# Optimization experiments

Hardware: AMD Instinct MI355X
Metric: run time of the kernel (lower is better)

## Reference

```python
import jax, jax.numpy as jnp
import numpy as np

N, E = 100000, 3200000
F_IN, H, ED, C = 21, 64, 3, 2
EPS = 1e-5


def setup_inputs() -> dict:
    key = jax.random.key(0)
    ks = jax.random.split(key, 20)
    def lin(k, fan_out, fan_in):
        s = 1.0 / np.sqrt(fan_in)
        return jax.random.uniform(k, (fan_out, fan_in), jnp.float32, -s, s)
    inp = {
        'x': jax.random.normal(ks[0], (N, F_IN), jnp.float32),
        'edge_index': jax.random.randint(ks[1], (2, E), 0, N, jnp.int64),
        'edge_attr': jax.random.normal(ks[2], (E, ED), jnp.float32),
        # edge encoder Linear(ED -> H)
        'We': lin(ks[3], H, ED), 'be': jnp.zeros((H,), jnp.float32),
        # conv1 SAGEConv(F_IN -> H): lin_l (neighbors, with bias), lin_r (root, no bias)
        'W1l': lin(ks[4], H, F_IN), 'b1l': jnp.zeros((H,), jnp.float32),
        'W1r': lin(ks[5], H, F_IN),
        # conv2 SAGEConv(H -> H)
        'W2l': lin(ks[6], H, H), 'b2l': jnp.zeros((H,), jnp.float32),
        'W2r': lin(ks[7], H, H),
        # BatchNorms
        'g1': jnp.ones((H,), jnp.float32), 'beta1': jnp.zeros((H,), jnp.float32),
        'g2': jnp.ones((H,), jnp.float32), 'beta2': jnp.zeros((H,), jnp.float32),
        # classifier Linear(H -> C)
        'Wc': lin(ks[8], C, H), 'bc': jnp.zeros((C,), jnp.float32),
    }
    return inp


def _bn(h, g, b):
    # training-mode BatchNorm1d: batch stats, biased variance
    mu = jnp.mean(h, axis=0)
    var = jnp.mean(jnp.square(h - mu), axis=0)
    return (h - mu) * jax.lax.rsqrt(var + EPS) * g + b


def reference(x, edge_index, edge_attr, We, be, W1l, b1l, W1r, W2l, b2l, W2r,
              g1, beta1, g2, beta2, Wc, bc):
    n = x.shape[0]
    src, dst = edge_index[0], edge_index[1]
    # degree (in-degree at target), clamped to 1 for mean aggregation
    deg = jax.ops.segment_sum(jnp.ones((src.shape[0],), x.dtype), dst, num_segments=n)
    inv_deg = (1.0 / jnp.maximum(deg, 1.0))[:, None]  # [N,1]

    def sage(h, Wl, bl, Wr):
        agg = jax.ops.segment_sum(h[src], dst, num_segments=n) * inv_deg  # mean over in-neighbors
        return agg @ Wl.T + bl + h @ Wr.T

    # edge feature encoding + scatter-add to target nodes
    edge_enc = jax.nn.relu(edge_attr @ We.T + be)                # [E,H]
    edge_agg = jax.ops.segment_sum(edge_enc, dst, num_segments=n)  # [N,H]

    h = sage(x, W1l, b1l, W1r) + edge_agg
    h = jax.nn.relu(_bn(h, g1, beta1))
    # dropout omitted (deterministic reference)
    h = sage(h, W2l, b2l, W2r)
    h = jax.nn.relu(_bn(h, g2, beta2))
    return h @ Wc.T + bc  # logits [N,2]
```

## Files before the change

### kernel.cpp

```cpp
#include <hip/hip_runtime.h>
#include <hip/hip_fp16.h>

#define NN 100000
#define NE 3200000
#define F_IN 21
#define HID 64
#define EPS 1e-5f

#define NB 1000
#define BN 100
#define SCAP 3712
#define AB 256
#define AEPB 12500


__global__ void __launch_bounds__(256) kC1_slab_r14(
    const int* __restrict__ src, const int* __restrict__ dst,
    const float* __restrict__ eattr,
    int* __restrict__ segStart, int* __restrict__ btot,
    float4* __restrict__ packB, unsigned char* __restrict__ dlArr) {
    __shared__ int lcnt[NB];
    __shared__ int lpart[256];
    __shared__ int lcur[NB];
    int tid = threadIdx.x;
    for (int i = tid; i < NB; i += 256) lcnt[i] = 0;
    __syncthreads();
    int base = blockIdx.x * AEPB;
    for (int k = tid; k < AEPB; k += 256) atomicAdd(&lcnt[dst[base + k] / BN], 1);
    __syncthreads();
    int mySum = 0;
    if (tid < 250)
        mySum = lcnt[4 * tid] + lcnt[4 * tid + 1] + lcnt[4 * tid + 2] + lcnt[4 * tid + 3];
    lpart[tid] = mySum;
    __syncthreads();
    for (int off = 1; off < 256; off <<= 1) {
        int v = (tid >= off) ? lpart[tid - off] : 0;
        __syncthreads();
        lpart[tid] += v;
        __syncthreads();
    }
    if (tid < 250) {
        int run = lpart[tid] - mySum;
#pragma unroll
        for (int j = 0; j < 4; ++j) {
            int b = 4 * tid + j;
            int c = lcnt[b];
            int st = base + run;
            lcur[b] = st;
            segStart[b * AB + blockIdx.x] = st;
            if (c) atomicAdd(&btot[b], c);
            run += c;
        }
    }
    if (tid == 0) segStart[NB * AB + blockIdx.x] = base + AEPB;
    __syncthreads();
    for (int k = tid; k < AEPB; k += 256) {
        int e = base + k;
        int d = dst[e];
        int b = d / BN;
        int dl = d - b * BN;
        int pos = atomicAdd(&lcur[b], 1);
        size_t eb = (size_t)e * 3;
        float4 pk = {__int_as_float(src[e] | (dl << 17)),
                     eattr[eb], eattr[eb + 1], eattr[eb + 2]};
        packB[pos] = pk;
        dlArr[pos] = (unsigned char)dl;
    }
}

__global__ void kB2_scan_r14(const int* __restrict__ btot, int* __restrict__ bucketBase,
                             int* __restrict__ rowptr) {
    __shared__ int lds[1024];
    int t = threadIdx.x;
    int v = (t < NB) ? btot[t] : 0;
    lds[t] = v;
    __syncthreads();
    for (int off = 1; off < 1024; off <<= 1) {
        int u = (t >= off) ? lds[t - off] : 0;
        __syncthreads();
        lds[t] += u;
        __syncthreads();
    }
    if (t < NB) bucketBase[t] = lds[t] - v;
    if (t == 0) rowptr[NN] = NE;
}

__global__ void kP_pad_r14(const float* __restrict__ x, __half* __restrict__ xh) {
    int i = blockIdx.x * blockDim.x + threadIdx.x;
    int st = gridDim.x * blockDim.x;
    for (; i < NN * 32; i += st) {
        int n = i >> 5, c = i & 31;
        xh[i] = __float2half((c < F_IN) ? x[(size_t)n * F_IN + c] : 0.f);
    }
}


#define R3X(v) { v += __shfl_xor(v, 8); v += __shfl_xor(v, 16); v += __shfl_xor(v, 32); }
#define R2X(v) { v += __shfl_xor(v, 16); v += __shfl_xor(v, 32); }
#define PICK(v, kk) ((kk) == 0 ? (v).x : (kk) == 1 ? (v).y : (kk) == 2 ? (v).z : (v).w)

__global__ void __launch_bounds__(512, 1) kFuse_r14(
    const float4* __restrict__ packB, const unsigned char* __restrict__ dlArr,
    const int* __restrict__ segStart, const int* __restrict__ bucketBase,
    const __half* __restrict__ xh, const float* __restrict__ x,
    const float* __restrict__ We, const float* __restrict__ be,
    const float* __restrict__ W1l, const float* __restrict__ b1l,
    const float* __restrict__ W1r,
    float* __restrict__ H1, int* __restrict__ csr_src, int* __restrict__ rowptr,
    float* __restrict__ gsum, float* __restrict__ gsq) {
    __shared__ float4 stage[SCAP];
    __shared__ int segA[AB], segL[AB];
    __shared__ int lcnt2[BN], lofs[BN], lcur2[BN];
    __shared__ float eLds[8 * HID];
    __shared__ float bs[HID], bq[HID];
    int tid = threadIdx.x;
    int b = blockIdx.x;
    int base = bucketBase[b];
    if (tid < AB) {
        int a = segStart[b * AB + tid];
        segA[tid] = a;
        segL[tid] = segStart[(b + 1) * AB + tid] - a;
    }
    for (int i = tid; i < BN; i += 512) lcnt2[i] = 0;
    if (tid < HID) { bs[tid] = 0.f; bq[tid] = 0.f; }
    __syncthreads();
    int lane = tid & 63, wid = tid >> 6;
    for (int s = wid; s < AB; s += 8) {
        int L = segL[s], A = segA[s];
        for (int i = lane; i < L; i += 64) atomicAdd(&lcnt2[dlArr[A + i]], 1);
    }
    __syncthreads();
    if (tid == 0) {
        int run = 0;
        for (int d = 0; d < BN; ++d) { lofs[d] = run; lcur2[d] = run; run += lcnt2[d]; }
    }
    __syncthreads();
    if (tid < BN) rowptr[b * BN + tid] = base + lofs[tid];
    for (int s = wid; s < AB; s += 8) {
        int L = segL[s], A = segA[s];
        for (int i = lane; i < L; i += 64) {
            float4 pk = packB[A + i];
            int dl = __float_as_int(pk.x) >> 17;
            int pos = atomicAdd(&lcur2[dl], 1);
            if (pos < SCAP) stage[pos] = pk;
        }
    }
    __syncthreads();
    int cntB = lofs[BN - 1] + lcnt2[BN - 1];
    int lim = min(cntB, SCAP);
    for (int i = tid; i < lim; i += 512)
        csr_src[base + i] = __float_as_int(stage[i].x) & 0x1FFFF;
    int g = lane >> 3, q = lane & 7;
    float w0[8], w1[8], w2[8], bqv[8];
#pragma unroll
    for (int r = 0; r < 8; ++r) {
        int ch = 8 * q + r;
        w0[r] = We[ch * 3]; w1[r] = We[ch * 3 + 1]; w2[r] = We[ch * 3 + 2];
        bqv[r] = be[ch];
    }
    float wl[F_IN], wr[F_IN];
#pragma unroll
    for (int k = 0; k < F_IN; ++k) {
        wl[k] = W1l[lane * F_IN + k];
        wr[k] = W1r[lane * F_IN + k];
    }
    float b1 = b1l[lane];
    float psum = 0.f, psq = 0.f;
    for (int d = wid; d < BN; d += 8) {
        int lbeg = lofs[d];
        int deg = lcnt2[d];
        int lend = lbeg + deg;
        float aX0 = 0, aX1 = 0, aX2 = 0, aX3 = 0;
        float aE[8] = {0, 0, 0, 0, 0, 0, 0, 0};
        for (int i0 = lbeg + g; i0 < lend; i0 += 32) {
            uint2 xv[4];
            float4 pk_[4];
            float mk[4];
#pragma unroll
            for (int u = 0; u < 4; ++u) {
                int i = i0 + u * 8;
                mk[u] = (i < lend) ? 1.f : 0.f;
                int ic = min(min(i, lend - 1), SCAP - 1);
                float4 pk = stage[ic];
                pk_[u] = pk;
                int s = __float_as_int(pk.x) & 0x1FFFF;
                xv[u] = *(const uint2*)(xh + (size_t)s * 32 + 4 * q);
            }
#pragma unroll
            for (int u = 0; u < 4; ++u) {
                float2 f0 = __half22float2(*(__half2*)&xv[u].x);
                float2 f1 = __half22float2(*(__half2*)&xv[u].y);
                float m = mk[u];
                aX0 = fmaf(f0.x, m, aX0);
                aX1 = fmaf(f0.y, m, aX1);
                aX2 = fmaf(f1.x, m, aX2);
                aX3 = fmaf(f1.y, m, aX3);
#pragma unroll
                for (int r = 0; r < 8; ++r) {
                    float e = fmaf(w0[r], pk_[u].y,
                              fmaf(w1[r], pk_[u].z, fmaf(w2[r], pk_[u].w, bqv[r])));
                    aE[r] = fmaf(fmaxf(e, 0.f), m, aE[r]);
                }
            }
        }
        R3X(aX0) R3X(aX1) R3X(aX2) R3X(aX3)
#pragma unroll
        for (int r = 0; r < 8; ++r) { R3X(aE[r]) }
        if (g == 0) {
            float4 e0 = {aE[0], aE[1], aE[2], aE[3]};
            float4 e1 = {aE[4], aE[5], aE[6], aE[7]};
            *(float4*)(eLds + wid * HID + 8 * q) = e0;
            *(float4*)(eLds + wid * HID + 8 * q + 4) = e1;
        }
        int n = b * BN + d;
        float4 aXq = {aX0, aX1, aX2, aX3};
        float xv = (lane < F_IN) ? x[(size_t)n * F_IN + lane] : 0.f;
        float own = b1, agg = 0.f;
#pragma unroll
        for (int k = 0; k < F_IN; ++k) {
            own = fmaf(wr[k], __shfl(xv, k), own);
            agg = fmaf(wl[k], __shfl(PICK(aXq, k & 3), k >> 2), agg);
        }
        float invd = 1.f / fmaxf((float)deg, 1.f);
        float h = own + agg * invd + eLds[wid * HID + lane];
        H1[(size_t)n * HID + lane] = h;
        psum += h; psq += h * h;
    }
    atomicAdd(&bs[lane], psum);
    atomicAdd(&bq[lane], psq);
    __syncthreads();
    if (tid < HID) {
        atomicAdd(&gsum[tid], bs[tid]);
        atomicAdd(&gsq[tid], bq[tid]);
    }
}

__global__ void kG_bnstat_r14(const float* __restrict__ gsum, const float* __restrict__ gsq,
                              const float* __restrict__ g, const float* __restrict__ beta,
                              float* __restrict__ scale, float* __restrict__ shift) {
    int c = threadIdx.x;
    if (c < HID) {
        float mu = gsum[c] * (1.f / (float)NN);
        float var = gsq[c] * (1.f / (float)NN) - mu * mu;
        float rstd = rsqrtf(var + EPS);
        float sc = rstd * g[c];
        scale[c] = sc;
        shift[c] = beta[c] - mu * sc;
    }
}

__global__ void kAct_r14(const float* __restrict__ H1,
                         const float* __restrict__ sc1, const float* __restrict__ sh1,
                         __half* __restrict__ act) {
    int i = blockIdx.x * blockDim.x + threadIdx.x;
    int st = gridDim.x * blockDim.x;
    for (; i < NN * HID; i += st) {
        int c = i & 63;
        act[i] = __float2half(fmaxf(fmaf(H1[i], sc1[c], sh1[c]), 0.f));
    }
}


__global__ void __launch_bounds__(256, 2) kG2f_r14(
    const __half* __restrict__ act, const int* __restrict__ csr_src,
    const int* __restrict__ rowptr,
    const float* __restrict__ W2l, const float* __restrict__ W2r,
    const float* __restrict__ b2l,
    float* __restrict__ h2, float* __restrict__ gsum, float* __restrict__ gsq) {
    __shared__ float ldsL[HID * HID];
    __shared__ float ldsR[HID * HID];
    __shared__ float bs[HID], bq[HID];
    for (int i = threadIdx.x; i < HID * HID; i += blockDim.x) {
        int k = i >> 6, c = i & 63;
        ldsL[i] = W2l[c * HID + k];
        ldsR[i] = W2r[c * HID + k];
    }
    if (threadIdx.x < HID) { bs[threadIdx.x] = 0.f; bq[threadIdx.x] = 0.f; }
    __syncthreads();
    int lane = threadIdx.x & 63;
    int g = lane >> 4, c4 = lane & 15;
    float b2 = b2l[lane];
    int gw = blockIdx.x * 4 + (threadIdx.x >> 6);
    int nw = gridDim.x * 4;
    float psum = 0.f, psq = 0.f;
    for (int n = gw; n < NN; n += nw) {
        int beg = rowptr[n], end = rowptr[n + 1];
        int deg = end - beg;
        float a0 = 0, a1 = 0, a2 = 0, a3 = 0;
        for (int p0 = beg; p0 < end; p0 += 64) {
            int cnt = min(64, end - p0);
            int sL = (lane < cnt) ? csr_src[p0 + lane] : 0;
            int jm = (cnt + 3) >> 2;
            for (int jb = 0; jb < jm; jb += 8) {
                uint2 v[8];
                float mk[8];
#pragma unroll
                for (int u = 0; u < 8; ++u) {
                    int idx = (jb + u) * 4 + g;
                    int s = __shfl(sL, idx);
                    mk[u] = (idx < cnt) ? 1.f : 0.f;
                    v[u] = *(const uint2*)(act + (size_t)s * HID + 4 * c4);
                }
#pragma unroll
                for (int u = 0; u < 8; ++u) {
                    float2 f0 = __half22float2(*(__half2*)&v[u].x);
                    float2 f1 = __half22float2(*(__half2*)&v[u].y);
                    float m = mk[u];
                    a0 = fmaf(f0.x, m, a0);
                    a1 = fmaf(f0.y, m, a1);
                    a2 = fmaf(f1.x, m, a2);
                    a3 = fmaf(f1.y, m, a3);
                }
            }
        }
        R2X(a0) R2X(a1) R2X(a2) R2X(a3)
        float invd = 1.f / fmaxf((float)deg, 1.f);
        float4 aq = {a0 * invd, a1 * invd, a2 * invd, a3 * invd};
        float v2 = __half2float(act[(size_t)n * HID + lane]);
        float o0 = b2, o1 = 0.f, o2 = 0.f, o3 = 0.f;
#pragma unroll
        for (int k = 0; k < HID; k += 4) {
            float va0 = __shfl(PICK(aq, k & 3), k >> 2);
            float vb0 = __shfl(v2, k);
            o0 = fmaf(ldsL[k * HID + lane], va0, fmaf(ldsR[k * HID + lane], vb0, o0));
            float va1 = __shfl(PICK(aq, (k + 1) & 3), (k + 1) >> 2);
            float vb1 = __shfl(v2, k + 1);
            o1 = fmaf(ldsL[(k + 1) * HID + lane], va1, fmaf(ldsR[(k + 1) * HID + lane], vb1, o1));
            float va2 = __shfl(PICK(aq, (k + 2) & 3), (k + 2) >> 2);
            float vb2 = __shfl(v2, k + 2);
            o2 = fmaf(ldsL[(k + 2) * HID + lane], va2, fmaf(ldsR[(k + 2) * HID + lane], vb2, o2));
            float va3 = __shfl(PICK(aq, (k + 3) & 3), (k + 3) >> 2);
            float vb3 = __shfl(v2, k + 3);
            o3 = fmaf(ldsL[(k + 3) * HID + lane], va3, fmaf(ldsR[(k + 3) * HID + lane], vb3, o3));
        }
        float o = (o0 + o1) + (o2 + o3);
        h2[(size_t)n * HID + lane] = o;
        psum += o; psq += o * o;
    }
    atomicAdd(&bs[lane], psum);
    atomicAdd(&bq[lane], psq);
    __syncthreads();
    if (threadIdx.x < HID) {
        atomicAdd(&gsum[threadIdx.x], bs[threadIdx.x]);
        atomicAdd(&gsq[threadIdx.x], bq[threadIdx.x]);
    }
}


__global__ void kJ_out_r14(const float* __restrict__ H2,
                           const float* __restrict__ sc2, const float* __restrict__ sh2,
                           const float* __restrict__ Wc, const float* __restrict__ bc,
                           float* __restrict__ out) {
    int lane = threadIdx.x & 63;
    int g = lane >> 4, c4 = lane & 15;
    int wv = blockIdx.x * 4 + (threadIdx.x >> 6);
    int nw = gridDim.x * 4;
    float4 sc = *(const float4*)(sc2 + 4 * c4);
    float4 sh = *(const float4*)(sh2 + 4 * c4);
    float4 w0 = *(const float4*)(Wc + 4 * c4);
    float4 w1 = *(const float4*)(Wc + HID + 4 * c4);
    float b0 = bc[0], b1 = bc[1];
    for (int t = wv; t < NN / 4; t += nw) {
        int n = t * 4 + g;
        float4 h = *(const float4*)(H2 + (size_t)n * HID + 4 * c4);
        float vx = fmaxf(fmaf(h.x, sc.x, sh.x), 0.f);
        float vy = fmaxf(fmaf(h.y, sc.y, sh.y), 0.f);
        float vz = fmaxf(fmaf(h.z, sc.z, sh.z), 0.f);
        float vw = fmaxf(fmaf(h.w, sc.w, sh.w), 0.f);
        float r0 = vx * w0.x + vy * w0.y + vz * w0.z + vw * w0.w;
        float r1 = vx * w1.x + vy * w1.y + vz * w1.z + vw * w1.w;
#pragma unroll
        for (int off = 1; off <= 8; off <<= 1) {
            r0 += __shfl_xor(r0, off);
            r1 += __shfl_xor(r1, off);
        }
        if (c4 == 0) {
            out[(size_t)n * 2] = r0 + b0;
            out[(size_t)n * 2 + 1] = r1 + b1;
        }
    }
}


extern "C" void kernel_launch(void* const* d_in, const int* in_sizes, int n_in,
                              void* d_out, int out_size, void* d_ws, size_t ws_size,
                              hipStream_t stream) {
    const float* x = (const float*)d_in[0];
    const int* ei = (const int*)d_in[1];
    const float* eattr = (const float*)d_in[2];
    const float* We = (const float*)d_in[3];
    const float* be = (const float*)d_in[4];
    const float* W1l = (const float*)d_in[5];
    const float* b1l = (const float*)d_in[6];
    const float* W1r = (const float*)d_in[7];
    const float* W2l = (const float*)d_in[8];
    const float* b2l = (const float*)d_in[9];
    const float* W2r = (const float*)d_in[10];
    const float* g1 = (const float*)d_in[11];
    const float* beta1 = (const float*)d_in[12];
    const float* g2 = (const float*)d_in[13];
    const float* beta2 = (const float*)d_in[14];
    const float* Wc = (const float*)d_in[15];
    const float* bc = (const float*)d_in[16];
    float* out = (float*)d_out;

    const int* e_src = ei;
    const int* e_dst = ei + NE;

    char* ws = (char*)d_ws;
    size_t off = 0;
    auto alloc = [&](size_t b) {
        char* p = ws + off;
        off += (b + 255) & ~(size_t)255;
        return p;
    };
    int* rowptr = (int*)alloc((NN + 1) * sizeof(int));
    int* segStart = (int*)alloc((size_t)(NB + 1) * AB * sizeof(int));
    int* btot = (int*)alloc(NB * sizeof(int));
    int* bucketBase = (int*)alloc(NB * sizeof(int));
    float4* packB = (float4*)alloc((size_t)NE * 16);
    unsigned char* dlArr = (unsigned char*)alloc((size_t)NE);
    int* csr_src = (int*)alloc((size_t)NE * sizeof(int));
    __half* xh = (__half*)alloc((size_t)NN * 32 * sizeof(__half));
    float* H1 = (float*)alloc((size_t)NN * HID * sizeof(float));
    __half* act = (__half*)alloc((size_t)NN * HID * sizeof(__half));
    float* stats = (float*)alloc(512 * sizeof(float));
    float* gsum1 = stats, *gsq1 = stats + 64, *gsum2 = stats + 128, *gsq2 = stats + 192;
    float* scale1 = stats + 256, *shift1 = stats + 320;
    float* scale2 = stats + 384, *shift2 = stats + 448;

    float* h2 = (float*)packB;

    hipMemsetAsync(btot, 0, NB * sizeof(int), stream);
    hipMemsetAsync(stats, 0, 256 * sizeof(float), stream);

    kC1_slab_r14<<<AB, 256, 0, stream>>>(e_src, e_dst, eattr, segStart, btot, packB, dlArr);
    kB2_scan_r14<<<1, 1024, 0, stream>>>(btot, bucketBase, rowptr);
    kP_pad_r14<<<1024, 256, 0, stream>>>(x, xh);
    kFuse_r14<<<NB, 512, 0, stream>>>(packB, dlArr, segStart, bucketBase,
                                      xh, x, We, be, W1l, b1l, W1r,
                                      H1, csr_src, rowptr, gsum1, gsq1);
    kG_bnstat_r14<<<1, 64, 0, stream>>>(gsum1, gsq1, g1, beta1, scale1, shift1);
    kAct_r14<<<2048, 256, 0, stream>>>(H1, scale1, shift1, act);
    kG2f_r14<<<2048, 256, 0, stream>>>(act, csr_src, rowptr, W2l, W2r, b2l,
                                       h2, gsum2, gsq2);
    kG_bnstat_r14<<<1, 64, 0, stream>>>(gsum2, gsq2, g2, beta2, scale2, shift2);
    kJ_out_r14<<<512, 256, 0, stream>>>(h2, scale2, shift2, Wc, bc, out);
}
```

Measured before the change: 580.5 us.

## Compress LDS edge staging to half, fold BN stats into consumers, retune grids

```diff
diff --git a/kernel.cpp b/kernel.cpp
--- a/kernel.cpp
+++ b/kernel.cpp
@@ -14,7 +14,7 @@
 #define AEPB 12500
 
 
-__global__ void __launch_bounds__(256) kC1_slab_r14(
+__global__ void __launch_bounds__(256) kC1_slab_r15(
     const int* __restrict__ src, const int* __restrict__ dst,
     const float* __restrict__ eattr,
     int* __restrict__ segStart, int* __restrict__ btot,
@@ -68,7 +68,7 @@
     }
 }
 
-__global__ void kB2_scan_r14(const int* __restrict__ btot, int* __restrict__ bucketBase,
+__global__ void kB2_scan_r15(const int* __restrict__ btot, int* __restrict__ bucketBase,
                              int* __restrict__ rowptr) {
     __shared__ int lds[1024];
     int t = threadIdx.x;
@@ -85,7 +85,7 @@
     if (t == 0) rowptr[NN] = NE;
 }
 
-__global__ void kP_pad_r14(const float* __restrict__ x, __half* __restrict__ xh) {
+__global__ void kP_pad_r15(const float* __restrict__ x, __half* __restrict__ xh) {
     int i = blockIdx.x * blockDim.x + threadIdx.x;
     int st = gridDim.x * blockDim.x;
     for (; i < NN * 32; i += st) {
@@ -99,7 +99,7 @@
 #define R2X(v) { v += __shfl_xor(v, 16); v += __shfl_xor(v, 32); }
 #define PICK(v, kk) ((kk) == 0 ? (v).x : (kk) == 1 ? (v).y : (kk) == 2 ? (v).z : (v).w)
 
-__global__ void __launch_bounds__(512, 1) kFuse_r14(
+__global__ void __launch_bounds__(512) kFuse_r15(
     const float4* __restrict__ packB, const unsigned char* __restrict__ dlArr,
     const int* __restrict__ segStart, const int* __restrict__ bucketBase,
     const __half* __restrict__ xh, const float* __restrict__ x,
@@ -108,7 +108,8 @@
     const float* __restrict__ W1r,
     float* __restrict__ H1, int* __restrict__ csr_src, int* __restrict__ rowptr,
     float* __restrict__ gsum, float* __restrict__ gsq) {
-    __shared__ float4 stage[SCAP];
+    __shared__ uint2 stageU[SCAP];
+    __shared__ unsigned short stageB[SCAP];
     __shared__ int segA[AB], segL[AB];
     __shared__ int lcnt2[BN], lofs[BN], lcur2[BN];
     __shared__ float eLds[8 * HID];
@@ -140,16 +141,22 @@
         int L = segL[s], A = segA[s];
         for (int i = lane; i < L; i += 64) {
             float4 pk = packB[A + i];
-            int dl = __float_as_int(pk.x) >> 17;
+            int enc = __float_as_int(pk.x);
+            int dl = enc >> 17;
             int pos = atomicAdd(&lcur2[dl], 1);
-            if (pos < SCAP) stage[pos] = pk;
+            if (pos < SCAP) {
+                __half2 h01 = __floats2half2_rn(pk.y, pk.z);
+                uint2 u = {(unsigned int)enc, *(unsigned int*)&h01};
+                stageU[pos] = u;
+                stageB[pos] = __half_as_ushort(__float2half(pk.w));
+            }
         }
     }
     __syncthreads();
     int cntB = lofs[BN - 1] + lcnt2[BN - 1];
     int lim = min(cntB, SCAP);
     for (int i = tid; i < lim; i += 512)
-        csr_src[base + i] = __float_as_int(stage[i].x) & 0x1FFFF;
+        csr_src[base + i] = (int)(stageU[i].x & 0x1FFFF);
     int g = lane >> 3, q = lane & 7;
     float w0[8], w1[8], w2[8], bqv[8];
 #pragma unroll
@@ -174,22 +181,24 @@
         float aE[8] = {0, 0, 0, 0, 0, 0, 0, 0};
         for (int i0 = lbeg + g; i0 < lend; i0 += 32) {
             uint2 xv[4];
-            float4 pk_[4];
+            uint2 su[4];
+            float a2f[4];
             float mk[4];
 #pragma unroll
             for (int u = 0; u < 4; ++u) {
                 int i = i0 + u * 8;
                 mk[u] = (i < lend) ? 1.f : 0.f;
                 int ic = min(min(i, lend - 1), SCAP - 1);
-                float4 pk = stage[ic];
-                pk_[u] = pk;
-                int s = __float_as_int(pk.x) & 0x1FFFF;
+                su[u] = stageU[ic];
+                a2f[u] = __half2float(__ushort_as_half(stageB[ic]));
+                int s = (int)(su[u].x & 0x1FFFF);
                 xv[u] = *(const uint2*)(xh + (size_t)s * 32 + 4 * q);
             }
 #pragma unroll
             for (int u = 0; u < 4; ++u) {
                 float2 f0 = __half22float2(*(__half2*)&xv[u].x);
                 float2 f1 = __half22float2(*(__half2*)&xv[u].y);
+                float2 a01 = __half22float2(*(__half2*)&su[u].y);
                 float m = mk[u];
                 aX0 = fmaf(f0.x, m, aX0);
                 aX1 = fmaf(f0.y, m, aX1);
@@ -197,8 +206,8 @@
                 aX3 = fmaf(f1.y, m, aX3);
 #pragma unroll
                 for (int r = 0; r < 8; ++r) {
-                    float e = fmaf(w0[r], pk_[u].y,
-                              fmaf(w1[r], pk_[u].z, fmaf(w2[r], pk_[u].w, bqv[r])));
+                    float e = fmaf(w0[r], a01.x,
+                              fmaf(w1[r], a01.y, fmaf(w2[r], a2f[u], bqv[r])));
                     aE[r] = fmaf(fmaxf(e, 0.f), m, aE[r]);
                 }
             }
@@ -235,33 +244,30 @@
     }
 }
 
-__global__ void kG_bnstat_r14(const float* __restrict__ gsum, const float* __restrict__ gsq,
-                              const float* __restrict__ g, const float* __restrict__ beta,
-                              float* __restrict__ scale, float* __restrict__ shift) {
-    int c = threadIdx.x;
-    if (c < HID) {
-        float mu = gsum[c] * (1.f / (float)NN);
-        float var = gsq[c] * (1.f / (float)NN) - mu * mu;
-        float rstd = rsqrtf(var + EPS);
-        float sc = rstd * g[c];
-        scale[c] = sc;
-        shift[c] = beta[c] - mu * sc;
-    }
-}
-
-__global__ void kAct_r14(const float* __restrict__ H1,
-                         const float* __restrict__ sc1, const float* __restrict__ sh1,
-                         __half* __restrict__ act) {
-    int i = blockIdx.x * blockDim.x + threadIdx.x;
+__global__ void kActB_r15(const float* __restrict__ H1,
+                          const float* __restrict__ gsum, const float* __restrict__ gsq,
+                          const float* __restrict__ g1, const float* __restrict__ beta1,
+                          __half* __restrict__ act) {
+    __shared__ float sc[HID], sh[HID];
+    int t = threadIdx.x;
+    if (t < HID) {
+        float mu = gsum[t] * (1.f / (float)NN);
+        float var = gsq[t] * (1.f / (float)NN) - mu * mu;
+        float s = rsqrtf(var + EPS) * g1[t];
+        sc[t] = s;
+        sh[t] = beta1[t] - mu * s;
+    }
+    __syncthreads();
+    int i = blockIdx.x * blockDim.x + t;
     int st = gridDim.x * blockDim.x;
     for (; i < NN * HID; i += st) {
         int c = i & 63;
-        act[i] = __float2half(fmaxf(fmaf(H1[i], sc1[c], sh1[c]), 0.f));
-    }
-}
-
-
-__global__ void __launch_bounds__(256, 2) kG2f_r14(
+        act[i] = __float2half(fmaxf(fmaf(H1[i], sc[c], sh[c]), 0.f));
+    }
+}
+
+
+__global__ void __launch_bounds__(256, 2) kG2f_r15(
     const __half* __restrict__ act, const int* __restrict__ csr_src,
     const int* __restrict__ rowptr,
     const float* __restrict__ W2l, const float* __restrict__ W2r,
@@ -347,21 +353,32 @@
 }
 
 
-__global__ void kJ_out_r14(const float* __restrict__ H2,
-                           const float* __restrict__ sc2, const float* __restrict__ sh2,
+__global__ void kJ_out_r15(const float* __restrict__ H2,
+                           const float* __restrict__ gsum, const float* __restrict__ gsq,
+                           const float* __restrict__ g2, const float* __restrict__ beta2,
                            const float* __restrict__ Wc, const float* __restrict__ bc,
                            float* __restrict__ out) {
-    int lane = threadIdx.x & 63;
+    __shared__ float scL[HID], shL[HID];
+    int t = threadIdx.x;
+    if (t < HID) {
+        float mu = gsum[t] * (1.f / (float)NN);
+        float var = gsq[t] * (1.f / (float)NN) - mu * mu;
+        float s = rsqrtf(var + EPS) * g2[t];
+        scL[t] = s;
+        shL[t] = beta2[t] - mu * s;
+    }
+    __syncthreads();
+    int lane = t & 63;
     int g = lane >> 4, c4 = lane & 15;
-    int wv = blockIdx.x * 4 + (threadIdx.x >> 6);
+    int wv = blockIdx.x * 4 + (t >> 6);
     int nw = gridDim.x * 4;
-    float4 sc = *(const float4*)(sc2 + 4 * c4);
-    float4 sh = *(const float4*)(sh2 + 4 * c4);
+    float4 sc = *(const float4*)(scL + 4 * c4);
+    float4 sh = *(const float4*)(shL + 4 * c4);
     float4 w0 = *(const float4*)(Wc + 4 * c4);
     float4 w1 = *(const float4*)(Wc + HID + 4 * c4);
     float b0 = bc[0], b1 = bc[1];
-    for (int t = wv; t < NN / 4; t += nw) {
-        int n = t * 4 + g;
+    for (int tt = wv; tt < NN / 4; tt += nw) {
+        int n = tt * 4 + g;
         float4 h = *(const float4*)(H2 + (size_t)n * HID + 4 * c4);
         float vx = fmaxf(fmaf(h.x, sc.x, sh.x), 0.f);
         float vy = fmaxf(fmaf(h.y, sc.y, sh.y), 0.f);
@@ -424,26 +441,22 @@
     __half* xh = (__half*)alloc((size_t)NN * 32 * sizeof(__half));
     float* H1 = (float*)alloc((size_t)NN * HID * sizeof(float));
     __half* act = (__half*)alloc((size_t)NN * HID * sizeof(__half));
-    float* stats = (float*)alloc(512 * sizeof(float));
+    float* stats = (float*)alloc(256 * sizeof(float));
     float* gsum1 = stats, *gsq1 = stats + 64, *gsum2 = stats + 128, *gsq2 = stats + 192;
-    float* scale1 = stats + 256, *shift1 = stats + 320;
-    float* scale2 = stats + 384, *shift2 = stats + 448;
 
     float* h2 = (float*)packB;
 
     hipMemsetAsync(btot, 0, NB * sizeof(int), stream);
     hipMemsetAsync(stats, 0, 256 * sizeof(float), stream);
 
-    kC1_slab_r14<<<AB, 256, 0, stream>>>(e_src, e_dst, eattr, segStart, btot, packB, dlArr);
-    kB2_scan_r14<<<1, 1024, 0, stream>>>(btot, bucketBase, rowptr);
-    kP_pad_r14<<<1024, 256, 0, stream>>>(x, xh);
-    kFuse_r14<<<NB, 512, 0, stream>>>(packB, dlArr, segStart, bucketBase,
+    kC1_slab_r15<<<AB, 256, 0, stream>>>(e_src, e_dst, eattr, segStart, btot, packB, dlArr);
+    kB2_scan_r15<<<1, 1024, 0, stream>>>(btot, bucketBase, rowptr);
+    kP_pad_r15<<<1024, 256, 0, stream>>>(x, xh);
+    kFuse_r15<<<NB, 512, 0, stream>>>(packB, dlArr, segStart, bucketBase,
                                       xh, x, We, be, W1l, b1l, W1r,
                                       H1, csr_src, rowptr, gsum1, gsq1);
-    kG_bnstat_r14<<<1, 64, 0, stream>>>(gsum1, gsq1, g1, beta1, scale1, shift1);
-    kAct_r14<<<2048, 256, 0, stream>>>(H1, scale1, shift1, act);
-    kG2f_r14<<<2048, 256, 0, stream>>>(act, csr_src, rowptr, W2l, W2r, b2l,
+    kActB_r15<<<2048, 256, 0, stream>>>(H1, gsum1, gsq1, g1, beta1, act);
+    kG2f_r15<<<4096, 256, 0, stream>>>(act, csr_src, rowptr, W2l, W2r, b2l,
                                        h2, gsum2, gsq2);
-    kG_bnstat_r14<<<1, 64, 0, stream>>>(gsum2, gsq2, g2, beta2, scale2, shift2);
-    kJ_out_r14<<<512, 256, 0, stream>>>(h2, scale2, shift2, Wc, bc, out);
-}
+    kJ_out_r15<<<512, 256, 0, stream>>>(h2, gsum2, gsq2, g2, beta2, Wc, bc, out);
+}
```

Result: slower. 604.9 us (+4.2%).
